# Performance work log

Measured on AMD Instinct MI355X. Metric: run time of the kernel, lower is better.

## Reference

```python
import jax, jax.numpy as jnp
import numpy as np

NX = 32; NY = 32; D = 2; K = 5; SCALE = 1.0
DX = 2.0 * SCALE / (NX - 1)
N = NX * NY

def _region_kernel():
    # kernel_size^d grid of offsets with spacing DX, centered at 0
    t = (jnp.arange(K, dtype=jnp.float32) - (K - 1) / 2.0) * DX
    gx, gy = jnp.meshgrid(t, t, indexing='ij')
    return jnp.stack((gx, gy), -1).reshape(-1, D)  # (K*K, 2)

def _build_cov(scaling, transform):
    # lower-triangular L: diag = scaling, strict lower = transform; cov = L L^T
    L = jnp.zeros((scaling.shape[0], D, D), scaling.dtype)
    L = L.at[:, 0, 0].set(scaling[:, 0])
    L = L.at[:, 1, 1].set(scaling[:, 1])
    L = L.at[:, 1, 0].set(transform[:, 0])
    return L @ jnp.swapaxes(L, -1, -2)

def reference(means, u, scaling, transform, conv_w, conv_b, emb_w, emb_b,
              lin1_w, lin1_b, sol_w, sol_b, tr_w, tr_b, sc_w, sc_b, tf_w, tf_b):
    cov = _build_cov(scaling, transform)          # (N,2,2)
    conics = jnp.linalg.inv(cov)                  # (N,2,2)
    # local sample gather: every Gaussian contributes K*K sample points
    samples = (means[:, None, :] + _region_kernel()[None]).reshape(-1, D)  # (S,2)
    # global Gaussian mixture evaluation at all sample points (no_grad in torch)
    diff = samples[:, None, :] - means[None, :, :]            # (S,N,2)
    Cd = jnp.einsum('nde,sne->snd', conics, diff)             # (S,N,2)
    G = jnp.exp(-0.5 * jnp.einsum('snd,snd->sn', diff, Cd))   # (S,N) densities
    w = G * u[None, :, 0]                                     # (S,N)
    u_s = jnp.sum(w, -1, keepdims=True)                       # (S,1)
    # Hessian of mixture: sum_j w_j ((C_j d)(C_j d)^T - C_j)
    wc = w[..., None] * Cd
    uxx = jnp.einsum('snd,sne->sde', wc, Cd) - jnp.einsum('sn,nde->sde', w, conics)
    pde = (uxx[:, 0, 0] + uxx[:, 1, 1])[:, None]              # diffusion rhs = laplacian
    mask = jnp.all(jnp.abs(samples) < SCALE, -1)[:, None].astype(u.dtype)
    img = jnp.concatenate((u_s, pde, mask), -1)               # (S, 3)
    img = img.reshape(N, K * K, 3).transpose(0, 2, 1).reshape(N, 3, K, K)
    img = jax.lax.stop_gradient(img)  # torch computes samples under no_grad
    params = jnp.concatenate((means, u, scaling, transform), -1)  # (N,6)
    # 4 stacked Networks (solution, translation, scale, transform); conv kernel
    # spans the whole K x K patch so Conv2d reduces to a tensordot
    y = jnp.tanh(jnp.einsum('ichw,mochw->mio', img, conv_w) + conv_b[:, None, :])
    e = jnp.tanh(jnp.einsum('ip,mpq->miq', params, emb_w) + emb_b[:, None, :])
    h = jnp.concatenate((y, e), -1)                               # (4,N,80)
    h = jnp.tanh(jnp.einsum('mio,moq->miq', h, lin1_w) + lin1_b[:, None, :])
    u_new = u + (h[0] @ sol_w + sol_b)
    means_new = means + (h[1] @ tr_w + tr_b)
    scaling_new = scaling * jnp.exp(h[2] @ sc_w + sc_b)
    transform_new = transform + (h[3] @ tf_w + tf_b)
    return jnp.concatenate((u_new, means_new, scaling_new, transform_new), -1)  # (N,6)

def setup_inputs() -> dict:
    key = jax.random.key(0)
    ks = jax.random.split(key, 14)
    tx = jnp.linspace(-1.0, 1.0, NX, dtype=jnp.float32) * SCALE
    ty = jnp.linspace(-1.0, 1.0, NY, dtype=jnp.float32) * SCALE
    gx, gy = jnp.meshgrid(tx, ty, indexing='ij')
    means = jnp.stack((gx, gy), -1).reshape(-1, D)
    scaling = jnp.full((N, D), float(np.exp(-4.5)) * SCALE, dtype=jnp.float32)
    transform = jnp.zeros((N, 1), jnp.float32)
    # initial u: gaussian bump (as in the torch __init__ default branch)
    u = jnp.exp(-0.5 * (means ** 2).sum(-1) / (0.1 * SCALE))[:, None].astype(jnp.float32)
    def p(k, shape, s):
        return jax.random.normal(k, shape, jnp.float32) * s
    return {
        'means': means, 'u': u, 'scaling': scaling, 'transform': transform,
        'conv_w': p(ks[0], (4, 50, 3, K, K), 0.08), 'conv_b': p(ks[1], (4, 50), 0.02),
        'emb_w': p(ks[2], (4, 6, 30), 0.3), 'emb_b': p(ks[3], (4, 30), 0.02),
        'lin1_w': p(ks[4], (4, 80, 80), 0.1), 'lin1_b': p(ks[5], (4, 80), 0.02),
        'sol_w': p(ks[6], (80, 1), 0.1), 'sol_b': jnp.zeros((1,), jnp.float32),
        'tr_w': p(ks[7], (80, 2), 0.1), 'tr_b': jnp.zeros((2,), jnp.float32),
        'sc_w': p(ks[8], (80, 2), 0.1), 'sc_b': jnp.zeros((2,), jnp.float32),
        'tf_w': p(ks[9], (80, 1), 0.1), 'tf_b': jnp.zeros((1,), jnp.float32),
    }
```

## Files before the change

kernel.cpp:

```cpp
#include <hip/hip_runtime.h>
#include <math.h>


namespace {

constexpr int NG = 1024;
constexpr float DXF = 2.0f / 31.0f;
constexpr float NHALF_LOG2E = -0.72134752044448170367f;
constexpr float TWO_LOG2E   = 2.88539008177792681472f;
constexpr float LOG2E       = 1.44269504088896340736f;

__device__ __forceinline__ float fast_tanh(float x) {
  x = fminf(9.0f, fmaxf(-9.0f, x));
  float t = __builtin_amdgcn_exp2f(TWO_LOG2E * x);
  return (t - 1.0f) * __builtin_amdgcn_rcpf(t + 1.0f);
}

__global__ __launch_bounds__(256) void k_prep(
    const float* __restrict__ conv_w, float* __restrict__ cwT)
{
  int idx = blockIdx.x * 256 + threadIdx.x;
  if (idx < 4 * 75 * 50) {
    int m = idx / 3750, r = idx - m * 3750;
    int c = r / 50, o = r - c * 50;
    cwT[idx] = conv_w[(m * 50 + o) * 75 + c];
  }
}

__global__ __launch_bounds__(256) void k_fused(
    const float* __restrict__ means, const float* __restrict__ uu,
    const float* __restrict__ scaling, const float* __restrict__ transform,
    const float* __restrict__ cwT, const float* __restrict__ conv_b,
    const float* __restrict__ emb_w, const float* __restrict__ emb_b,
    const float* __restrict__ lin1_w, const float* __restrict__ lin1_b,
    const float* __restrict__ sol_w, const float* __restrict__ sol_b,
    const float* __restrict__ tr_w, const float* __restrict__ tr_b,
    const float* __restrict__ sc_w, const float* __restrict__ sc_b,
    const float* __restrict__ tf_w, const float* __restrict__ tf_b,
    float* __restrict__ out)
{
  __shared__ float4 gp[NG];
  __shared__ float2 gq[NG];
  __shared__ float r_us[10][25];
  __shared__ float r_pde[10][25];
  __shared__ float simg[75];
  __shared__ float sparams[6];
  __shared__ float h[320];
  __shared__ float h2[320];
  __shared__ float hpart[6][8];

  const int i = blockIdx.x;
  const int tid = threadIdx.x;

  for (int g = tid; g < NG; g += 256) {
    float mx = means[2 * g], my = means[2 * g + 1];
    float s0 = scaling[2 * g], s1 = scaling[2 * g + 1];
    float t0 = transform[g];
    float cc  = 1.0f / (s1 * s1);
    float is0 = 1.0f / s0;
    float bb  = -t0 * cc * is0;
    float aa  = (t0 * t0 * cc + 1.0f) * is0 * is0;
    gp[g] = make_float4(mx, my, aa, bb);
    gq[g] = make_float2(cc, uu[g]);
  }
  if (tid < 6) {
    float v;
    if (tid < 2)       v = means[2 * i + tid];
    else if (tid == 2) v = uu[i];
    else if (tid < 5)  v = scaling[2 * i + (tid - 3)];
    else               v = transform[i];
    sparams[tid] = v;
  }
  __syncthreads();

  if (tid < 250) {
    const int c = tid / 25;
    const int s = tid - c * 25;
    const int kx = s / 5, ky = s - kx * 5;
    const float sx = means[2 * i]     + (float)(kx - 2) * DXF;
    const float sy = means[2 * i + 1] + (float)(ky - 2) * DXF;
    const int base = (c < 4) ? 103 * c : 412 + 102 * (c - 4);
    const int len  = (c < 4) ? 103 : 102;
    float us = 0.0f, pde = 0.0f;
#pragma unroll 4
    for (int j = 0; j < len; ++j) {
      const int g = base + j;
      float4 p  = gp[g];
      float2 qv = gq[g];
      float dx = sx - p.x, dy = sy - p.y;
      float a = p.z, b = p.w, cc = qv.x;
      float Cd0 = a * dx + b * dy;
      float Cd1 = b * dx + cc * dy;
      float q   = dx * Cd0 + dy * Cd1;
      float w   = qv.y * __builtin_amdgcn_exp2f(NHALF_LOG2E * q);
      us  += w;
      pde += w * (Cd0 * Cd0 + Cd1 * Cd1 - (a + cc));
    }
    r_us[c][s]  = us;
    r_pde[c][s] = pde;
  }
  __syncthreads();

  if (tid < 25) {
    float U = 0.0f, P = 0.0f;
#pragma unroll
    for (int c = 0; c < 10; ++c) { U += r_us[c][tid]; P += r_pde[c][tid]; }
    const int kx = tid / 5, ky = tid - kx * 5;
    const float sx = sparams[0] + (float)(kx - 2) * DXF;
    const float sy = sparams[1] + (float)(ky - 2) * DXF;
    simg[tid]      = U;
    simg[25 + tid] = P;
    simg[50 + tid] = (fabsf(sx) < 1.0f && fabsf(sy) < 1.0f) ? 1.0f : 0.0f;
  }
  __syncthreads();

  if (tid < 200) {
    const int m = tid / 50, o = tid - m * 50;
    const float* w = cwT + m * 3750 + o;
    float acc = conv_b[m * 50 + o];
#pragma unroll
    for (int c = 0; c < 75; ++c) acc = fmaf(simg[c], w[c * 50], acc);
    h[m * 80 + o] = fast_tanh(acc);
  }
  if (tid >= 200) {
    for (int e = tid - 200; e < 120; e += 56) {
      const int m = e / 30, q = e - m * 30;
      float acc = emb_b[m * 30 + q];
#pragma unroll
      for (int p = 0; p < 6; ++p) acc = fmaf(sparams[p], emb_w[(m * 6 + p) * 30 + q], acc);
      h[m * 80 + 50 + q] = fast_tanh(acc);
    }
  }
  __syncthreads();

  for (int idx = tid; idx < 320; idx += 256) {
    const int m = idx / 80, q = idx - m * 80;
    const float* lw = lin1_w + m * 6400 + q;
    const float* hh = h + m * 80;
    float acc = lin1_b[m * 80 + q];
#pragma unroll 8
    for (int j = 0; j < 80; ++j) acc = fmaf(hh[j], lw[j * 80], acc);
    h2[idx] = fast_tanh(acc);
  }
  __syncthreads();

  if (tid < 48) {
    const int o = tid >> 3, c8 = tid & 7;
    const int m = (o == 0) ? 0 : (o < 3) ? 1 : (o < 5) ? 2 : 3;
    const float* wp; int stride;
    if (o == 0)      { wp = sol_w;            stride = 1; }
    else if (o < 3)  { wp = tr_w + (o - 1);   stride = 2; }
    else if (o < 5)  { wp = sc_w + (o - 3);   stride = 2; }
    else             { wp = tf_w;             stride = 1; }
    const float* hh = h2 + m * 80;
    float acc = 0.0f;
    const int j0 = c8 * 10;
#pragma unroll
    for (int j = 0; j < 10; ++j) acc = fmaf(hh[j0 + j], wp[(j0 + j) * stride], acc);
    hpart[o][c8] = acc;
  }
  __syncthreads();

  if (tid < 6) {
    float acc = 0.0f;
#pragma unroll
    for (int c = 0; c < 8; ++c) acc += hpart[tid][c];
    float res;
    if (tid == 0)      res = sparams[2] + acc + sol_b[0];
    else if (tid < 3)  res = sparams[tid - 1] + acc + tr_b[tid - 1];
    else if (tid < 5)  res = sparams[tid] * __builtin_amdgcn_exp2f(LOG2E * (acc + sc_b[tid - 3]));
    else               res = sparams[5] + acc + tf_b[0];
    out[i * 6 + tid] = res;
  }
}

}

extern "C" void kernel_launch(void* const* d_in, const int* in_sizes, int n_in,
                              void* d_out, int out_size, void* d_ws, size_t ws_size,
                              hipStream_t stream) {
  const float* means     = (const float*)d_in[0];
  const float* uu        = (const float*)d_in[1];
  const float* scaling   = (const float*)d_in[2];
  const float* transform = (const float*)d_in[3];
  const float* conv_w    = (const float*)d_in[4];
  const float* conv_b    = (const float*)d_in[5];
  const float* emb_w     = (const float*)d_in[6];
  const float* emb_b     = (const float*)d_in[7];
  const float* lin1_w    = (const float*)d_in[8];
  const float* lin1_b    = (const float*)d_in[9];
  const float* sol_w     = (const float*)d_in[10];
  const float* sol_b     = (const float*)d_in[11];
  const float* tr_w      = (const float*)d_in[12];
  const float* tr_b      = (const float*)d_in[13];
  const float* sc_w      = (const float*)d_in[14];
  const float* sc_b      = (const float*)d_in[15];
  const float* tf_w      = (const float*)d_in[16];
  const float* tf_b      = (const float*)d_in[17];

  float* cwT = (float*)d_ws;
  float* out = (float*)d_out;

  k_prep<<<59, 256, 0, stream>>>(conv_w, cwT);
  k_fused<<<1024, 256, 0, stream>>>(means, uu, scaling, transform,
                                    cwT, conv_b, emb_w, emb_b, lin1_w, lin1_b,
                                    sol_w, sol_b, tr_w, tr_b, sc_w, sc_b, tf_w, tf_b,
                                    out);
}
```

Baseline: 111.9 us.

## Cull distant Gaussians per block before mixture evaluation

Each block now filters the Gaussians, keeping only those whose distance from the 5x5 sample patch is within a bound scaled by the covariance trace. Survivors are compacted into shared memory with an atomic counter, and the density loop runs over just that list. This removes most of the exp and FMA work per sample, since the Gaussians are narrow. In exchange it adds shared atomics and a data-dependent loop count. The result also becomes approximate, because contributions past the cutoff are dropped (exp(-40) or smaller), and the bound uses the trace as a proxy for the largest eigenvalue, which may not hold for arbitrary inputs.

Measured after the change: 101.8 us. -9.0%, faster.

```diff
diff --git a/kernel.cpp b/kernel.cpp
--- a/kernel.cpp
+++ b/kernel.cpp
@@ -9,6 +9,7 @@
 constexpr float NHALF_LOG2E = -0.72134752044448170367f;
 constexpr float TWO_LOG2E   = 2.88539008177792681472f;
 constexpr float LOG2E       = 1.44269504088896340736f;
+constexpr float QCUT        = 80.0f;
 
 __device__ __forceinline__ float fast_tanh(float x) {
   x = fminf(9.0f, fmaxf(-9.0f, x));
@@ -39,8 +40,9 @@
     const float* __restrict__ tf_w, const float* __restrict__ tf_b,
     float* __restrict__ out)
 {
-  __shared__ float4 gp[NG];
-  __shared__ float2 gq[NG];
+  __shared__ float4 sgp[NG];
+  __shared__ float2 sgq[NG];
+  __shared__ int s_cnt;
   __shared__ float r_us[10][25];
   __shared__ float r_pde[10][25];
   __shared__ float simg[75];
@@ -52,17 +54,7 @@
   const int i = blockIdx.x;
   const int tid = threadIdx.x;
 
-  for (int g = tid; g < NG; g += 256) {
-    float mx = means[2 * g], my = means[2 * g + 1];
-    float s0 = scaling[2 * g], s1 = scaling[2 * g + 1];
-    float t0 = transform[g];
-    float cc  = 1.0f / (s1 * s1);
-    float is0 = 1.0f / s0;
-    float bb  = -t0 * cc * is0;
-    float aa  = (t0 * t0 * cc + 1.0f) * is0 * is0;
-    gp[g] = make_float4(mx, my, aa, bb);
-    gq[g] = make_float2(cc, uu[g]);
-  }
+  if (tid == 0) s_cnt = 0;
   if (tid < 6) {
     float v;
     if (tid < 2)       v = means[2 * i + tid];
@@ -73,20 +65,37 @@
   }
   __syncthreads();
 
+  const float mxi = sparams[0], myi = sparams[1];
+  for (int g = tid; g < NG; g += 256) {
+    float gmx = means[2 * g], gmy = means[2 * g + 1];
+    float s0 = scaling[2 * g], s1 = scaling[2 * g + 1];
+    float t0 = transform[g];
+    float ex = fmaxf(fabsf(gmx - mxi) - 2.0f * DXF, 0.0f);
+    float ey = fmaxf(fabsf(gmy - myi) - 2.0f * DXF, 0.0f);
+    float tr = s0 * s0 + s1 * s1 + t0 * t0;
+    if (ex * ex + ey * ey <= QCUT * tr) {
+      int idx = atomicAdd(&s_cnt, 1);
+      float cc  = 1.0f / (s1 * s1);
+      float is0 = 1.0f / s0;
+      float bb  = -t0 * cc * is0;
+      float aa  = (t0 * t0 * cc + 1.0f) * is0 * is0;
+      sgp[idx] = make_float4(gmx, gmy, aa, bb);
+      sgq[idx] = make_float2(cc, uu[g]);
+    }
+  }
+  __syncthreads();
+
+  const int cnt = s_cnt;
   if (tid < 250) {
     const int c = tid / 25;
     const int s = tid - c * 25;
     const int kx = s / 5, ky = s - kx * 5;
-    const float sx = means[2 * i]     + (float)(kx - 2) * DXF;
-    const float sy = means[2 * i + 1] + (float)(ky - 2) * DXF;
-    const int base = (c < 4) ? 103 * c : 412 + 102 * (c - 4);
-    const int len  = (c < 4) ? 103 : 102;
+    const float sx = mxi + (float)(kx - 2) * DXF;
+    const float sy = myi + (float)(ky - 2) * DXF;
     float us = 0.0f, pde = 0.0f;
-#pragma unroll 4
-    for (int j = 0; j < len; ++j) {
-      const int g = base + j;
-      float4 p  = gp[g];
-      float2 qv = gq[g];
+    for (int j = c; j < cnt; j += 10) {
+      float4 p  = sgp[j];
+      float2 qv = sgq[j];
       float dx = sx - p.x, dy = sy - p.y;
       float a = p.z, b = p.w, cc = qv.x;
       float Cd0 = a * dx + b * dy;
@@ -106,8 +115,8 @@
 #pragma unroll
     for (int c = 0; c < 10; ++c) { U += r_us[c][tid]; P += r_pde[c][tid]; }
     const int kx = tid / 5, ky = tid - kx * 5;
-    const float sx = sparams[0] + (float)(kx - 2) * DXF;
-    const float sy = sparams[1] + (float)(ky - 2) * DXF;
+    const float sx = mxi + (float)(kx - 2) * DXF;
+    const float sy = myi + (float)(ky - 2) * DXF;
     simg[tid]      = U;
     simg[25 + tid] = P;
     simg[50 + tid] = (fabsf(sx) < 1.0f && fabsf(sy) < 1.0f) ? 1.0f : 0.0f;
```
